# Optimization experiments

Hardware: AMD Instinct MI355X
Metric: run time of the kernel (lower is better)

## Reference

```python
import jax, jax.numpy as jnp
import numpy as np

T, K, D, CIN = 8, 64, 512, 1536  # timesteps, num_centers, redu_dim, input channels


def _conv(x, w, b=None, pad=0):
    y = jax.lax.conv_general_dilated(x, w, (1, 1), [(pad, pad), (pad, pad)],
                                     dimension_numbers=('NCHW', 'OIHW', 'NCHW'))
    return y if b is None else y + b[None, :, None, None]


def setup_inputs() -> dict:
    key = jax.random.key(0)
    ks = jax.random.split(key, 15)
    B, H, W = 32, 8, 8
    s = lambda i, shp: jax.random.normal(ks[i], shp, jnp.float32) * 0.05
    return dict(
        x=jax.random.normal(ks[0], (B * T, CIN, H, W), jnp.float32),
        redu_w=s(1, (D, CIN, 1, 1)), redu_b=s(2, (D,)),
        w_x=s(3, (K, D, 1, 1)),
        att_x=s(4, (K, K, 3, 3)), att_h_w=s(5, (K, K, 3, 3)), att_b=s(6, (K,)),
        share_w=s(7, (K, K, 3, 3)), share_b=s(8, (K,)),
        U_r=s(9, (K, K, 3, 3)), U_z=s(10, (K, K, 3, 3)), U_h=s(11, (K, K, 3, 3)),
        centers=s(12, (K, D)),
        fc1_w=s(13, (T * K // 16, T * K)), fc2_w=s(14, (T * K, T * K // 16)),
    )


def reference(x, redu_w, redu_b, w_x, att_x, att_h_w, att_b, share_w, share_b,
              U_r, U_z, U_h, centers, fc1_w, fc2_w):
    NT, _, H, W = x.shape
    B = NT // T
    xt = _conv(x, redu_w, redu_b)                    # (B*T, D, H, W) 1x1 reduction
    wxpb = _conv(xt, w_x)                            # (B*T, K, H, W)
    att_v = _conv(wxpb, att_x, pad=1).reshape(B, T, K, H, W).transpose(1, 0, 2, 3, 4)  # (T,B,K,H,W)
    wxpb5 = wxpb.reshape(B, T, K, H, W)

    def fc(v):  # ChannelAttention shared MLP (1x1 convs == matmuls)
        return jnp.maximum(v @ fc1_w.T, 0.) @ fc2_w.T

    def step(h, _):
        ah = _conv(h, att_h_w, att_b, pad=1)               # (B,K,H,W)
        e = jax.nn.relu(att_v + ah[None])                  # (T,B,K,H,W)
        e = e.transpose(1, 0, 2, 3, 4).reshape(B, T * K, H * W)
        g = jnp.tanh(fc(e.mean(-1)) + fc(e.max(-1)))       # (B, T*K) channel attention
        ex = jnp.exp(g.reshape(B, T, K))
        den = ex.sum(1, keepdims=True)
        den = den + (den == 0).astype(ex.dtype)
        alphas = ex / den                                  # softmax over timesteps
        wxt = (alphas[:, :, :, None, None] * wxpb5).sum(1) # (B,K,H,W)
        wxt = _conv(wxt, share_w, share_b, pad=1)
        z = jax.nn.sigmoid(wxt + _conv(h, U_z, pad=1))
        r = jax.nn.sigmoid(wxt + _conv(h, U_r, pad=1))
        hh = jnp.tanh(wxt + _conv(r * h, U_h, pad=1))
        h_new = (1. - z) * hh + z * h
        return h_new, h_new

    h0 = jnp.zeros((B, K, H, W), x.dtype)
    _, hs = jax.lax.scan(step, h0, None, length=T)         # (T,B,K,H,W)
    assigns = hs.transpose(1, 0, 2, 3, 4).reshape(B * T, K, H * W)
    a_sum = assigns.sum(-1, keepdims=True)                 # (B*T,K,1)
    a = a_sum * centers[None]                              # (B*T,K,D)
    feats = xt.reshape(B * T, D, H * W).transpose(0, 2, 1) # (B*T,HW,D)
    vlad = jnp.einsum('nks,nsd->nkd', assigns, feats) - a  # (B*T,K,D)
    vlad = vlad.reshape(B, T, K, D).sum(1)                 # (B,K,D)
    vlad = vlad / jnp.maximum(jnp.linalg.norm(vlad, axis=2, keepdims=True), 1e-12)
    vlad = vlad.reshape(B, K * D)
    vlad = vlad / jnp.maximum(jnp.linalg.norm(vlad, axis=1, keepdims=True), 1e-12)
    return vlad
```

## Files before the change

kernel.cpp:

```cpp
#include <hip/hip_runtime.h>
#include <math.h>

#define T_   8
#define K_   64
#define D_   512
#define CIN_ 1536
#define B_   32
#define S_   64
#define NT_  256

#define WLO_BF16  786432u
#define WXT_OFF   786432u
#define XT_OFF    819200u
#define WXPB_OFF  9207808u
#define ATTV_OFF  10256384u
#define HS_OFF    11436032u
#define ASUM_OFF  13041664u
#define WPB       25034752u

typedef __bf16 v8bf __attribute__((ext_vector_type(8)));
typedef __bf16 v4bf __attribute__((ext_vector_type(4)));
typedef float  v4f  __attribute__((ext_vector_type(4)));
typedef _Float16 v4h __attribute__((ext_vector_type(4)));
typedef _Float16 v8h __attribute__((ext_vector_type(8)));

__global__ __launch_bounds__(256) void k_prep(const float* __restrict__ redu_w,
                                              const float* __restrict__ w_x,
                                              float* __restrict__ ws) {
    unsigned idx = blockIdx.x * 256u + threadIdx.x;
    if (idx < 786432u) {
        float f = redu_w[idx];
        __bf16 h = (__bf16)f;
        __bf16 l = (__bf16)(f - (float)h);
        __bf16* wb = (__bf16*)ws;
        wb[idx] = h;
        wb[WLO_BF16 + idx] = l;
    } else if (idx < 819200u) {
        unsigned i = idx - 786432u;
        unsigned dd = i >> 6, k = i & 63u;
        ws[WXT_OFF + i] = w_x[k * 512u + dd];
    }
}

__global__ __launch_bounds__(256) void k_prep_w(const float* __restrict__ w0,
                                                const float* __restrict__ w1,
                                                const float* __restrict__ w2,
                                                const float* __restrict__ w3,
                                                const float* __restrict__ w4,
                                                float* __restrict__ ws) {
    unsigned idx = blockIdx.x * 256u + threadIdx.x;
    if (idx >= 184320u) return;
    unsigned w = idx / 36864u, r = idx % 36864u;
    const float* src = (w == 0) ? w0 : (w == 1) ? w1 : (w == 2) ? w2 : (w == 3) ? w3 : w4;
    float f = src[r];
    __bf16 h = (__bf16)f;
    __bf16 l = (__bf16)(f - (float)h);
    unsigned o = r / 576u, rem = r % 576u, ii = rem / 9u, dydx = rem % 9u;
    __bf16* wb = (__bf16*)ws;
    unsigned dst = WPB + w * 73728u + (dydx * 64u + o) * 64u + ii;
    wb[dst] = h;
    wb[dst + 36864u] = l;
}

__global__ __launch_bounds__(256) void k_gemm_xt_mfma(const float* __restrict__ x,
                                                      const float* __restrict__ redu_b,
                                                      float* __restrict__ ws) {
    __shared__ __bf16 xhi_s[64 * 72];
    __shared__ __bf16 xlo_s[64 * 72];
    const __bf16* __restrict__ Whi = (const __bf16*)ws;
    const __bf16* __restrict__ Wlo = ((const __bf16*)ws) + WLO_BF16;
    float* xt = ws + XT_OFF;
    const int n = blockIdx.y;
    const int d0 = blockIdx.x * 256;
    const int tid = threadIdx.x;
    const int wave = tid >> 6, lane = tid & 63;
    const int lrow = lane & 15, lkg = lane >> 4;
    const int m_base = d0 + wave * 64;
    const float* __restrict__ xn = x + n * 98304;
    const int s4 = tid & 15, cb = tid >> 4;

    v4f acc[4][4];
#pragma unroll
    for (int mt = 0; mt < 4; ++mt)
#pragma unroll
        for (int nt = 0; nt < 4; ++nt) acc[mt][nt] = (v4f){0.f, 0.f, 0.f, 0.f};

    for (int c0 = 0; c0 < 1536; c0 += 64) {
        float4 v[4];
#pragma unroll
        for (int j = 0; j < 4; ++j)
            v[j] = *(const float4*)&xn[(c0 + cb * 4 + j) * 64 + s4 * 4];
        __syncthreads();
#pragma unroll
        for (int i = 0; i < 4; ++i) {
            v4bf hv, lv;
#pragma unroll
            for (int j = 0; j < 4; ++j) {
                float f = ((const float*)&v[j])[i];
                __bf16 h = (__bf16)f;
                hv[j] = h;
                lv[j] = (__bf16)(f - (float)h);
            }
            int row = s4 * 4 + i;
            *(v4bf*)&xhi_s[row * 72 + cb * 4] = hv;
            *(v4bf*)&xlo_s[row * 72 + cb * 4] = lv;
        }
        __syncthreads();
#pragma unroll
        for (int ks = 0; ks < 64; ks += 32) {
            v8bf bh[4], bl[4], ah[4], al[4];
#pragma unroll
            for (int nt = 0; nt < 4; ++nt) {
                int off = (nt * 16 + lrow) * 72 + ks + lkg * 8;
                bh[nt] = *(const v8bf*)&xhi_s[off];
                bl[nt] = *(const v8bf*)&xlo_s[off];
            }
#pragma unroll
            for (int mt = 0; mt < 4; ++mt) {
                int gi = (m_base + mt * 16 + lrow) * 1536 + c0 + ks + lkg * 8;
                ah[mt] = *(const v8bf*)&Whi[gi];
                al[mt] = *(const v8bf*)&Wlo[gi];
            }
#pragma unroll
            for (int mt = 0; mt < 4; ++mt)
#pragma unroll
                for (int nt = 0; nt < 4; ++nt) {
                    acc[mt][nt] = __builtin_amdgcn_mfma_f32_16x16x32_bf16(
                        ah[mt], bh[nt], acc[mt][nt], 0, 0, 0);
                    acc[mt][nt] = __builtin_amdgcn_mfma_f32_16x16x32_bf16(
                        ah[mt], bl[nt], acc[mt][nt], 0, 0, 0);
                    acc[mt][nt] = __builtin_amdgcn_mfma_f32_16x16x32_bf16(
                        al[mt], bh[nt], acc[mt][nt], 0, 0, 0);
                }
        }
    }
#pragma unroll
    for (int mt = 0; mt < 4; ++mt) {
#pragma unroll
        for (int r = 0; r < 4; ++r) {
            int m = m_base + mt * 16 + lkg * 4 + r;
            float bias = redu_b[m];
#pragma unroll
            for (int nt = 0; nt < 4; ++nt) {
                int s = nt * 16 + lrow;
                xt[(n * 512 + m) * 64 + s] = acc[mt][nt][r] + bias;
            }
        }
    }
}

__global__ __launch_bounds__(256) void k_gemm_wxpb(float* __restrict__ ws) {
    __shared__ float Aw[16 * 64];
    __shared__ float Bx[16 * 64];
    const float* wxT = ws + WXT_OFF;
    const float* xt = ws + XT_OFF;
    float* wxpb = ws + WXPB_OFF;
    const int n = blockIdx.x;
    const int tid = threadIdx.x;
    const int sg = tid & 15, kg = tid >> 4;

    float acc[4][4];
#pragma unroll
    for (int i = 0; i < 4; ++i)
#pragma unroll
        for (int j = 0; j < 4; ++j) acc[i][j] = 0.f;

    for (int d0 = 0; d0 < 512; d0 += 16) {
        int cc = tid >> 4, q = tid & 15;
        *(float4*)&Aw[cc * 64 + q * 4] = *(const float4*)&wxT[(d0 + cc) * 64 + q * 4];
        *(float4*)&Bx[cc * 64 + q * 4] = *(const float4*)&xt[n * 32768 + (d0 + cc) * 64 + q * 4];
        __syncthreads();
#pragma unroll
        for (int c2 = 0; c2 < 16; ++c2) {
            float4 a = *(const float4*)&Aw[c2 * 64 + kg * 4];
            float4 b = *(const float4*)&Bx[c2 * 64 + sg * 4];
            float av[4] = {a.x, a.y, a.z, a.w};
            float bv[4] = {b.x, b.y, b.z, b.w};
#pragma unroll
            for (int i = 0; i < 4; ++i)
#pragma unroll
                for (int j = 0; j < 4; ++j)
                    acc[i][j] = fmaf(av[i], bv[j], acc[i][j]);
        }
        __syncthreads();
    }
#pragma unroll
    for (int i = 0; i < 4; ++i) {
        float4 o = {acc[i][0], acc[i][1], acc[i][2], acc[i][3]};
        *(float4*)&wxpb[(n * 64 + kg * 4 + i) * 64 + sg * 4] = o;
    }
}

__global__ __launch_bounds__(128) void k_conv3x3(const float* __restrict__ in,
                                                 const float* __restrict__ wt,
                                                 const float* __restrict__ bias,
                                                 float* __restrict__ out) {
    __shared__ float in_s[4096];
    __shared__ float w_s[16 * 576];
    const int img = blockIdx.y;
    const int k0 = blockIdx.x * 16;
    const int tid = threadIdx.x;
    const int kl = tid >> 3, y = tid & 7;
#pragma unroll
    for (int i = 0; i < 8; ++i) {
        int f = tid + i * 128;
        *(float4*)&in_s[f * 4] = *(const float4*)&in[img * 4096 + f * 4];
    }
#pragma unroll
    for (int i = 0; i < 18; ++i) {
        int f = tid + i * 128;
        *(float4*)&w_s[f * 4] = *(const float4*)&wt[k0 * 576 + f * 4];
    }
    __syncthreads();
    float o[8];
#pragma unroll
    for (int xx = 0; xx < 8; ++xx) o[xx] = 0.f;
    for (int kp = 0; kp < 64; ++kp) {
        const float* wp = &w_s[kl * 576 + kp * 9];
        float wv[9];
#pragma unroll
        for (int q = 0; q < 9; ++q) wv[q] = wp[q];
#pragma unroll
        for (int dy = 0; dy < 3; ++dy) {
            int yy = y + dy - 1;
            if (yy >= 0 && yy < 8) {
                float4 ra = *(const float4*)&in_s[kp * 64 + yy * 8];
                float4 rb = *(const float4*)&in_s[kp * 64 + yy * 8 + 4];
                float r[8] = {ra.x, ra.y, ra.z, ra.w, rb.x, rb.y, rb.z, rb.w};
                float wa = wv[dy * 3 + 0], wb = wv[dy * 3 + 1], wc = wv[dy * 3 + 2];
#pragma unroll
                for (int xx = 0; xx < 8; ++xx) {
                    float t = wb * r[xx];
                    if (xx > 0) t += wa * r[xx - 1];
                    if (xx < 7) t += wc * r[xx + 1];
                    o[xx] += t;
                }
            }
        }
    }
    float bv = bias ? bias[k0 + kl] : 0.f;
    float4 o0 = {o[0] + bv, o[1] + bv, o[2] + bv, o[3] + bv};
    float4 o1 = {o[4] + bv, o[5] + bv, o[6] + bv, o[7] + bv};
    *(float4*)&out[img * 4096 + (k0 + kl) * 64 + y * 8] = o0;
    *(float4*)&out[img * 4096 + (k0 + kl) * 64 + y * 8 + 4] = o1;
}

__device__ __forceinline__ void conv_mfma(const __bf16* __restrict__ Wh,
                                          const __bf16* tS,
                                          int l15, int kg8, int mt, int ntb,
                                          v4f acc[2]) {
    v8bf vz;
#pragma unroll
    for (int q = 0; q < 8; ++q) vz[q] = (__bf16)0.f;
    v4f a0 = (v4f){0.f, 0.f, 0.f, 0.f};
    v4f a1 = (v4f){0.f, 0.f, 0.f, 0.f};
    const int n0 = ntb * 16 + l15;
#pragma unroll
    for (int dy = 0; dy < 3; ++dy) {
        v8bf wh[3][2];
#pragma unroll
        for (int dx = 0; dx < 3; ++dx) {
            const int wrow = ((dy * 3 + dx) * 64 + mt * 16 + l15) * 64 + kg8;
#pragma unroll
            for (int kci = 0; kci < 2; ++kci)
                wh[dx][kci] = *(const v8bf*)&Wh[wrow + kci * 32];
        }
#pragma unroll
        for (int dx = 0; dx < 3; ++dx) {
            const int y0 = (n0 >> 3) + dy - 1, x0 = (n0 & 7) + dx - 1;
            const bool okx = (unsigned)x0 < 8u;
            const bool ok0 = ((unsigned)y0 < 8u) & okx;
            const bool ok1 = ((unsigned)(y0 + 2) < 8u) & okx;
            const int s0 = ((y0 * 8 + x0) & 63) * 72 + kg8;
            const int s1 = (((y0 + 2) * 8 + x0) & 63) * 72 + kg8;
#pragma unroll
            for (int kci = 0; kci < 2; ++kci) {
                v8bf b0 = ok0 ? *(const v8bf*)&tS[s0 + kci * 32] : vz;
                v8bf b1 = ok1 ? *(const v8bf*)&tS[s1 + kci * 32] : vz;
                a0 = __builtin_amdgcn_mfma_f32_16x16x32_bf16(wh[dx][kci], b0, a0, 0, 0, 0);
                a1 = __builtin_amdgcn_mfma_f32_16x16x32_bf16(wh[dx][kci], b1, a1, 0, 0, 0);
            }
        }
    }
    acc[0] = a0;
    acc[1] = a1;
}

__device__ __forceinline__ void write_c(float* c, const v4f acc[2],
                                        int l15, int kg, int mt, int ntb) {
#pragma unroll
    for (int i = 0; i < 2; ++i)
#pragma unroll
        for (int r = 0; r < 4; ++r)
            c[(mt * 16 + kg * 4 + r) * 65 + (ntb + i) * 16 + l15] = acc[i][r];
}

__attribute__((amdgpu_waves_per_eu(2)))
__global__ __launch_bounds__(512) void k_recur(const float* __restrict__ att_b,
                                               const float* __restrict__ share_b,
                                               const float* __restrict__ fc1_w,
                                               const float* __restrict__ fc2_w,
                                               float* __restrict__ ws) {
    __shared__ float h_s[4096];
    __shared__ __attribute__((aligned(16))) __bf16 tA[64 * 72];
    __shared__ float cA[64 * 65];
    __shared__ float cB[64 * 65];
    __shared__ float misc[1088];
    __shared__ __attribute__((aligned(16))) _Float16 attv_s[32768];
    const int b = blockIdx.x, tid = threadIdx.x;
    const int lane = tid & 63;
    const int wave = tid >> 6, mt = wave >> 1, ntb = (wave & 1) * 2;
    const int l15 = lane & 15, kg = lane >> 4, kg8 = kg * 8;
    const int kk = tid >> 3, yy = tid & 7;
    const __bf16* Wp = (const __bf16*)ws + WPB;
    const float* attv = ws + ATTV_OFF;
    const float* wxpb = ws + WXPB_OFF;
    float* hsg = ws + HS_OFF;
    float* asg = ws + ASUM_OFF;

    {
        const float* src = attv + b * 32768;
        for (int i = tid; i < 8192; i += 512) {
            float4 v = *(const float4*)&src[i * 4];
            v4h h4 = {(_Float16)v.x, (_Float16)v.y, (_Float16)v.z, (_Float16)v.w};
            *(v4h*)&attv_s[i * 4] = h4;
        }
    }
    float wxv[8][8];
    {
        const float* src = wxpb + b * 32768 + kk * 64 + yy * 8;
#pragma unroll
        for (int tp = 0; tp < 8; ++tp) {
            float4 a = *(const float4*)&src[tp * 4096];
            float4 c = *(const float4*)&src[tp * 4096 + 4];
            wxv[tp][0] = a.x; wxv[tp][1] = a.y; wxv[tp][2] = a.z; wxv[tp][3] = a.w;
            wxv[tp][4] = c.x; wxv[tp][5] = c.y; wxv[tp][6] = c.z; wxv[tp][7] = c.w;
        }
    }

    for (int i = tid; i < 4096; i += 512) h_s[i] = 0.f;
    const float abv = att_b[kk];
    float sb4[4];
#pragma unroll
    for (int r = 0; r < 4; ++r) sb4[r] = share_b[mt * 16 + kg * 4 + r];
    __syncthreads();

    for (int t = 0; t < 8; ++t) {
        {
            int s = tid & 63, g = tid >> 6;
#pragma unroll
            for (int q4 = 0; q4 < 2; ++q4) {
                v4bf hv;
#pragma unroll
                for (int q = 0; q < 4; ++q) hv[q] = (__bf16)h_s[(g * 8 + q4 * 4 + q) * 64 + s];
                *(v4bf*)&tA[s * 72 + g * 8 + q4 * 4] = hv;
            }
        }
        __syncthreads();
        {
            v4f a[2];
            conv_mfma(Wp, tA, l15, kg8, mt, ntb, a);
            write_c(cA, a, l15, kg, mt, ntb);
        }
        __syncthreads();
        {
            float ah8[8];
            const float* cr = &cA[kk * 65 + yy * 8];
#pragma unroll
            for (int xx = 0; xx < 8; ++xx) ah8[xx] = cr[xx] + abv;
            for (int tp = 0; tp < 8; ++tp) {
                v8h va = *(const v8h*)&attv_s[tp * 4096 + kk * 64 + yy * 8];
                float s_ = 0.f, m_ = 0.f;
#pragma unroll
                for (int xx = 0; xx < 8; ++xx) {
                    float v = fmaxf((float)va[xx] + ah8[xx], 0.f);
                    s_ += v;
                    m_ = fmaxf(m_, v);
                }
                s_ += __shfl_down(s_, 4, 8);
                s_ += __shfl_down(s_, 2, 8);
                s_ += __shfl_down(s_, 1, 8);
                m_ = fmaxf(m_, __shfl_down(m_, 4, 8));
                m_ = fmaxf(m_, __shfl_down(m_, 2, 8));
                m_ = fmaxf(m_, __shfl_down(m_, 1, 8));
                if (yy == 0) {
                    misc[tp * 64 + kk] = s_ * (1.f / 64.f);
                    misc[512 + tp * 64 + kk] = m_;
                }
            }
        }
        __syncthreads();
        {
            int i2 = tid >> 3, part = tid & 7;
            int i = i2 & 31;
            const float* src = misc + ((i2 < 32) ? 0 : 512);
            const float* wrow = fc1_w + i * 512 + part * 64;
            const float* s2 = src + part * 64;
            float p = 0.f;
#pragma unroll
            for (int c4 = 0; c4 < 16; ++c4) {
                float4 wv = *(const float4*)&wrow[c4 * 4];
                float4 sv = *(const float4*)&s2[c4 * 4];
                p = fmaf(wv.x, sv.x, p);
                p = fmaf(wv.y, sv.y, p);
                p = fmaf(wv.z, sv.z, p);
                p = fmaf(wv.w, sv.w, p);
            }
            p += __shfl_down(p, 4, 8);
            p += __shfl_down(p, 2, 8);
            p += __shfl_down(p, 1, 8);
            if (part == 0) misc[1024 + i2] = fmaxf(p, 0.f);
        }
        __syncthreads();
        {
            const float* w2 = fc2_w + tid * 32;
            float gm = 0.f, gx = 0.f;
#pragma unroll
            for (int i4 = 0; i4 < 8; ++i4) {
                float4 wv = *(const float4*)&w2[i4 * 4];
                gm = fmaf(wv.x, misc[1024 + i4 * 4 + 0], gm);
                gm = fmaf(wv.y, misc[1024 + i4 * 4 + 1], gm);
                gm = fmaf(wv.z, misc[1024 + i4 * 4 + 2], gm);
                gm = fmaf(wv.w, misc[1024 + i4 * 4 + 3], gm);
                gx = fmaf(wv.x, misc[1056 + i4 * 4 + 0], gx);
                gx = fmaf(wv.y, misc[1056 + i4 * 4 + 1], gx);
                gx = fmaf(wv.z, misc[1056 + i4 * 4 + 2], gx);
                gx = fmaf(wv.w, misc[1056 + i4 * 4 + 3], gx);
            }
            misc[tid] = expf(tanhf(gm + gx));
        }
        __syncthreads();
        {
            int k6 = tid & 63;
            float den = 0.f;
#pragma unroll
            for (int tp = 0; tp < 8; ++tp) den += misc[tp * 64 + k6];
            den += (den == 0.f) ? 1.f : 0.f;
            misc[512 + tid] = misc[tid] / den;
        }
        __syncthreads();
        float wx8[8];
        {
#pragma unroll
            for (int xx = 0; xx < 8; ++xx) wx8[xx] = 0.f;
#pragma unroll
            for (int tp = 0; tp < 8; ++tp) {
                float al = misc[512 + tp * 64 + kk];
#pragma unroll
                for (int xx = 0; xx < 8; ++xx) wx8[xx] = fmaf(al, wxv[tp][xx], wx8[xx]);
            }
        }
        v4f az[2], ar[2];
        conv_mfma(Wp + 2u * 73728u, tA, l15, kg8, mt, ntb, az);
        conv_mfma(Wp + 3u * 73728u, tA, l15, kg8, mt, ntb, ar);
        __syncthreads();
#pragma unroll
        for (int xx = 0; xx < 8; ++xx) tA[(yy * 8 + xx) * 72 + kk] = (__bf16)wx8[xx];
        __syncthreads();
        v4f ash[2];
        conv_mfma(Wp + 1u * 73728u, tA, l15, kg8, mt, ntb, ash);
        float zf[2][4], wof[2][4];
#pragma unroll
        for (int i = 0; i < 2; ++i)
#pragma unroll
            for (int r = 0; r < 4; ++r) {
                int ko = mt * 16 + kg * 4 + r;
                int s = (ntb + i) * 16 + l15;
                float wo = ash[i][r] + sb4[r];
                float z = 1.f / (1.f + expf(-(wo + az[i][r])));
                float rr = 1.f / (1.f + expf(-(wo + ar[i][r])));
                cB[ko * 65 + s] = rr * h_s[ko * 64 + s];
                zf[i][r] = z;
                wof[i][r] = wo;
            }
        __syncthreads();
        {
            int s = tid & 63, g = tid >> 6;
#pragma unroll
            for (int q4 = 0; q4 < 2; ++q4) {
                v4bf hv;
#pragma unroll
                for (int q = 0; q < 4; ++q) hv[q] = (__bf16)cB[(g * 8 + q4 * 4 + q) * 65 + s];
                *(v4bf*)&tA[s * 72 + g * 8 + q4 * 4] = hv;
            }
        }
        if (tid < 64) misc[1024 + tid] = 0.f;
        __syncthreads();
        v4f ach[2];
        conv_mfma(Wp + 4u * 73728u, tA, l15, kg8, mt, ntb, ach);
#pragma unroll
        for (int r = 0; r < 4; ++r) {
            int ko = mt * 16 + kg * 4 + r;
            float rsum = 0.f;
#pragma unroll
            for (int i = 0; i < 2; ++i) {
                int s = (ntb + i) * 16 + l15;
                float hh = tanhf(wof[i][r] + ach[i][r]);
                float hold = h_s[ko * 64 + s];
                float hn = (1.f - zf[i][r]) * hh + zf[i][r] * hold;
                h_s[ko * 64 + s] = hn;
                hsg[((t * 32 + b) * 64 + ko) * 64 + s] = hn;
                rsum += hn;
            }
            rsum += __shfl_xor(rsum, 8, 16);
            rsum += __shfl_xor(rsum, 4, 16);
            rsum += __shfl_xor(rsum, 2, 16);
            rsum += __shfl_xor(rsum, 1, 16);
            if (l15 == 0) atomicAdd(&misc[1024 + ko], rsum);
        }
        __syncthreads();
        if (tid < 64) asg[b * 512 + t * 64 + tid] = misc[1024 + tid];
        __syncthreads();
    }
}

__global__ __launch_bounds__(256) void k_vlad(const float* __restrict__ centers,
                                              const float* __restrict__ ws,
                                              float* __restrict__ out) {
    __shared__ float As[16 * 68];
    __shared__ float Bs[16 * 68];
    const int b = blockIdx.y;
    const int d0 = blockIdx.x * 64;
    const int tid = threadIdx.x;
    const int kq = tid & 15, dq = tid >> 4;
    const int lk = tid >> 2, q = tid & 3;
    const float* hs = ws + HS_OFF;
    const float* xt = ws + XT_OFF;
    float acc[4][4];
#pragma unroll
    for (int i = 0; i < 4; ++i)
#pragma unroll
        for (int j = 0; j < 4; ++j) acc[i][j] = 0.f;

    for (int rc = 0; rc < 512; rc += 16) {
        int t = rc >> 6, hw0 = rc & 63;
        float4 va = *(const float4*)&hs[((t * 32 + b) * 64 + lk) * 64 + hw0 + q * 4];
        float4 vb = *(const float4*)&xt[(b * 8 + t) * 32768 + (d0 + lk) * 64 + hw0 + q * 4];
        __syncthreads();
        As[(q * 4 + 0) * 68 + lk] = va.x;
        As[(q * 4 + 1) * 68 + lk] = va.y;
        As[(q * 4 + 2) * 68 + lk] = va.z;
        As[(q * 4 + 3) * 68 + lk] = va.w;
        Bs[(q * 4 + 0) * 68 + lk] = vb.x;
        Bs[(q * 4 + 1) * 68 + lk] = vb.y;
        Bs[(q * 4 + 2) * 68 + lk] = vb.z;
        Bs[(q * 4 + 3) * 68 + lk] = vb.w;
        __syncthreads();
#pragma unroll
        for (int cc = 0; cc < 16; ++cc) {
            float4 a = *(const float4*)&As[cc * 68 + kq * 4];
            float4 bb = *(const float4*)&Bs[cc * 68 + dq * 4];
            float av[4] = {a.x, a.y, a.z, a.w};
            float bv[4] = {bb.x, bb.y, bb.z, bb.w};
#pragma unroll
            for (int i = 0; i < 4; ++i)
#pragma unroll
                for (int j = 0; j < 4; ++j)
                    acc[i][j] = fmaf(av[i], bv[j], acc[i][j]);
        }
    }
    const float* asum = ws + ASUM_OFF;
#pragma unroll
    for (int i = 0; i < 4; ++i) {
        int k = kq * 4 + i;
        float at = 0.f;
#pragma unroll
        for (int tp = 0; tp < 8; ++tp) at += asum[b * 512 + tp * 64 + k];
        float4 cen = *(const float4*)&centers[k * 512 + d0 + dq * 4];
        float4 o = {acc[i][0] - at * cen.x, acc[i][1] - at * cen.y,
                    acc[i][2] - at * cen.z, acc[i][3] - at * cen.w};
        *(float4*)&out[b * 32768 + k * 512 + d0 + dq * 4] = o;
    }
}

__global__ __launch_bounds__(64) void k_norm1(float* __restrict__ out) {
    const int b = blockIdx.x >> 6, k = blockIdx.x & 63;
    float* p = out + b * 32768 + k * 512;
    const int tid = threadIdx.x;
    float v[8];
    float ss = 0.f;
#pragma unroll
    for (int i = 0; i < 8; ++i) {
        v[i] = p[tid + i * 64];
        ss = fmaf(v[i], v[i], ss);
    }
#pragma unroll
    for (int off = 32; off > 0; off >>= 1) ss += __shfl_down(ss, off, 64);
    ss = __shfl(ss, 0, 64);
    float sc = 1.f / fmaxf(sqrtf(ss), 1e-12f);
#pragma unroll
    for (int i = 0; i < 8; ++i) p[tid + i * 64] = v[i] * sc;
}

__global__ __launch_bounds__(256) void k_norm2(float* __restrict__ out) {
    __shared__ float red[4];
    __shared__ float stot;
    const int b = blockIdx.x;
    const int tid = threadIdx.x;
    float* p = out + b * 32768;
    float ss = 0.f;
    for (int i = 0; i < 32; ++i) {
        float4 v = *(const float4*)&p[tid * 4 + i * 1024];
        ss += v.x * v.x + v.y * v.y + v.z * v.z + v.w * v.w;
    }
#pragma unroll
    for (int off = 32; off > 0; off >>= 1) ss += __shfl_down(ss, off, 64);
    if ((tid & 63) == 0) red[tid >> 6] = ss;
    __syncthreads();
    if (tid == 0) stot = 1.f / fmaxf(sqrtf(red[0] + red[1] + red[2] + red[3]), 1e-12f);
    __syncthreads();
    float sc = stot;
    for (int i = 0; i < 32; ++i) {
        float4 v = *(const float4*)&p[tid * 4 + i * 1024];
        v.x *= sc; v.y *= sc; v.z *= sc; v.w *= sc;
        *(float4*)&p[tid * 4 + i * 1024] = v;
    }
}

extern "C" void kernel_launch(void* const* d_in, const int* in_sizes, int n_in,
                              void* d_out, int out_size, void* d_ws, size_t ws_size,
                              hipStream_t stream) {
    const float* x       = (const float*)d_in[0];
    const float* redu_w  = (const float*)d_in[1];
    const float* redu_b  = (const float*)d_in[2];
    const float* w_x     = (const float*)d_in[3];
    const float* att_x   = (const float*)d_in[4];
    const float* att_h_w = (const float*)d_in[5];
    const float* att_b   = (const float*)d_in[6];
    const float* share_w = (const float*)d_in[7];
    const float* share_b = (const float*)d_in[8];
    const float* U_r     = (const float*)d_in[9];
    const float* U_z     = (const float*)d_in[10];
    const float* U_h     = (const float*)d_in[11];
    const float* centers = (const float*)d_in[12];
    const float* fc1_w   = (const float*)d_in[13];
    const float* fc2_w   = (const float*)d_in[14];
    float* ws = (float*)d_ws;
    float* out = (float*)d_out;

    k_prep<<<dim3(3200), dim3(256), 0, stream>>>(redu_w, w_x, ws);
    k_prep_w<<<dim3(720), dim3(256), 0, stream>>>(att_h_w, share_w, U_z, U_r, U_h, ws);
    k_gemm_xt_mfma<<<dim3(2, 256), dim3(256), 0, stream>>>(x, redu_b, ws);
    k_gemm_wxpb<<<dim3(256), dim3(256), 0, stream>>>(ws);
    k_conv3x3<<<dim3(4, 256), dim3(128), 0, stream>>>(ws + WXPB_OFF, att_x,
                                                      (const float*)nullptr, ws + ATTV_OFF);
    k_recur<<<dim3(32), dim3(512), 0, stream>>>(att_b, share_b, fc1_w, fc2_w, ws);
    k_vlad<<<dim3(8, 32), dim3(256), 0, stream>>>(centers, ws, out);
    k_norm1<<<dim3(2048), dim3(64), 0, stream>>>(out);
    k_norm2<<<dim3(32), dim3(256), 0, stream>>>(out);
}
```

Before: 761.2 us.

## Fuse three h-convolutions into one MFMA pass and reload wxpb per step

```diff
diff --git a/kernel.cpp b/kernel.cpp
--- a/kernel.cpp
+++ b/kernel.cpp
@@ -286,6 +286,55 @@
     acc[1] = a1;
 }
 
+__device__ __forceinline__ void conv_mfma3(const __bf16* __restrict__ W0,
+                                           const __bf16* __restrict__ W1,
+                                           const __bf16* __restrict__ W2,
+                                           const __bf16* tS,
+                                           int l15, int kg8, int mt, int ntb,
+                                           v4f a0[2], v4f a1[2], v4f a2[2]) {
+    v8bf vz;
+#pragma unroll
+    for (int q = 0; q < 8; ++q) vz[q] = (__bf16)0.f;
+#pragma unroll
+    for (int i = 0; i < 2; ++i) {
+        a0[i] = (v4f){0.f, 0.f, 0.f, 0.f};
+        a1[i] = (v4f){0.f, 0.f, 0.f, 0.f};
+        a2[i] = (v4f){0.f, 0.f, 0.f, 0.f};
+    }
+    const int n0 = ntb * 16 + l15;
+#pragma unroll
+    for (int dy = 0; dy < 3; ++dy) {
+#pragma unroll
+        for (int dx = 0; dx < 3; ++dx) {
+            const int wrow = ((dy * 3 + dx) * 64 + mt * 16 + l15) * 64 + kg8;
+            v8bf w0[2], w1[2], w2[2];
+#pragma unroll
+            for (int kci = 0; kci < 2; ++kci) {
+                w0[kci] = *(const v8bf*)&W0[wrow + kci * 32];
+                w1[kci] = *(const v8bf*)&W1[wrow + kci * 32];
+                w2[kci] = *(const v8bf*)&W2[wrow + kci * 32];
+            }
+            const int y0 = (n0 >> 3) + dy - 1, x0 = (n0 & 7) + dx - 1;
+            const bool okx = (unsigned)x0 < 8u;
+            const bool ok0 = ((unsigned)y0 < 8u) & okx;
+            const bool ok1 = ((unsigned)(y0 + 2) < 8u) & okx;
+            const int s0 = ((y0 * 8 + x0) & 63) * 72 + kg8;
+            const int s1 = (((y0 + 2) * 8 + x0) & 63) * 72 + kg8;
+#pragma unroll
+            for (int kci = 0; kci < 2; ++kci) {
+                v8bf b0 = ok0 ? *(const v8bf*)&tS[s0 + kci * 32] : vz;
+                v8bf b1 = ok1 ? *(const v8bf*)&tS[s1 + kci * 32] : vz;
+                a0[0] = __builtin_amdgcn_mfma_f32_16x16x32_bf16(w0[kci], b0, a0[0], 0, 0, 0);
+                a0[1] = __builtin_amdgcn_mfma_f32_16x16x32_bf16(w0[kci], b1, a0[1], 0, 0, 0);
+                a1[0] = __builtin_amdgcn_mfma_f32_16x16x32_bf16(w1[kci], b0, a1[0], 0, 0, 0);
+                a1[1] = __builtin_amdgcn_mfma_f32_16x16x32_bf16(w1[kci], b1, a1[1], 0, 0, 0);
+                a2[0] = __builtin_amdgcn_mfma_f32_16x16x32_bf16(w2[kci], b0, a2[0], 0, 0, 0);
+                a2[1] = __builtin_amdgcn_mfma_f32_16x16x32_bf16(w2[kci], b1, a2[1], 0, 0, 0);
+            }
+        }
+    }
+}
+
 __device__ __forceinline__ void write_c(float* c, const v4f acc[2],
                                         int l15, int kg, int mt, int ntb) {
 #pragma unroll
@@ -295,7 +344,6 @@
             c[(mt * 16 + kg * 4 + r) * 65 + (ntb + i) * 16 + l15] = acc[i][r];
 }
 
-__attribute__((amdgpu_waves_per_eu(2)))
 __global__ __launch_bounds__(512) void k_recur(const float* __restrict__ att_b,
                                                const float* __restrict__ share_b,
                                                const float* __restrict__ fc1_w,
@@ -326,17 +374,6 @@
             *(v4h*)&attv_s[i * 4] = h4;
         }
     }
-    float wxv[8][8];
-    {
-        const float* src = wxpb + b * 32768 + kk * 64 + yy * 8;
-#pragma unroll
-        for (int tp = 0; tp < 8; ++tp) {
-            float4 a = *(const float4*)&src[tp * 4096];
-            float4 c = *(const float4*)&src[tp * 4096 + 4];
-            wxv[tp][0] = a.x; wxv[tp][1] = a.y; wxv[tp][2] = a.z; wxv[tp][3] = a.w;
-            wxv[tp][4] = c.x; wxv[tp][5] = c.y; wxv[tp][6] = c.z; wxv[tp][7] = c.w;
-        }
-    }
 
     for (int i = tid; i < 4096; i += 512) h_s[i] = 0.f;
     const float abv = att_b[kk];
@@ -357,9 +394,11 @@
             }
         }
         __syncthreads();
+        v4f az[2], ar[2];
         {
             v4f a[2];
-            conv_mfma(Wp, tA, l15, kg8, mt, ntb, a);
+            conv_mfma3(Wp, Wp + 2u * 73728u, Wp + 3u * 73728u, tA,
+                       l15, kg8, mt, ntb, a, az, ar);
             write_c(cA, a, l15, kg, mt, ntb);
         }
         __syncthreads();
@@ -439,23 +478,23 @@
             misc[512 + tid] = misc[tid] / den;
         }
         __syncthreads();
-        float wx8[8];
-        {
+        {
+            float wx8[8];
 #pragma unroll
             for (int xx = 0; xx < 8; ++xx) wx8[xx] = 0.f;
+            const float* src0 = wxpb + b * 32768 + kk * 64 + yy * 8;
 #pragma unroll
             for (int tp = 0; tp < 8; ++tp) {
                 float al = misc[512 + tp * 64 + kk];
-#pragma unroll
-                for (int xx = 0; xx < 8; ++xx) wx8[xx] = fmaf(al, wxv[tp][xx], wx8[xx]);
-            }
-        }
-        v4f az[2], ar[2];
-        conv_mfma(Wp + 2u * 73728u, tA, l15, kg8, mt, ntb, az);
-        conv_mfma(Wp + 3u * 73728u, tA, l15, kg8, mt, ntb, ar);
-        __syncthreads();
-#pragma unroll
-        for (int xx = 0; xx < 8; ++xx) tA[(yy * 8 + xx) * 72 + kk] = (__bf16)wx8[xx];
+                float4 v0 = *(const float4*)&src0[tp * 4096];
+                float4 v1 = *(const float4*)&src0[tp * 4096 + 4];
+                float v[8] = {v0.x, v0.y, v0.z, v0.w, v1.x, v1.y, v1.z, v1.w};
+#pragma unroll
+                for (int xx = 0; xx < 8; ++xx) wx8[xx] = fmaf(al, v[xx], wx8[xx]);
+            }
+#pragma unroll
+            for (int xx = 0; xx < 8; ++xx) tA[(yy * 8 + xx) * 72 + kk] = (__bf16)wx8[xx];
+        }
         __syncthreads();
         v4f ash[2];
         conv_mfma(Wp + 1u * 73728u, tA, l15, kg8, mt, ntb, ash);
```

New measurement: 752.0 us. No clear change (-1.2%).
